# Performance work log

Measured on AMD Instinct MI355X. Metric: run time of the kernel, lower is better.

The kernel has to match this reference:

```python
import jax, jax.numpy as jnp
import numpy as np

NUM_EMBEDDINGS = 1024
EMBEDDING_DIM = 256
COMMITMENT_COST = 0.25


def setup_inputs() -> dict:
    key = jax.random.key(0)
    k1, k2 = jax.random.split(key)
    z_e = jax.random.normal(k1, (32, EMBEDDING_DIM, 32, 32), dtype=jnp.float32)
    # nn.Embedding weight init: uniform(-1/K, 1/K)
    embedding = jax.random.uniform(
        k2, (NUM_EMBEDDINGS, EMBEDDING_DIM), dtype=jnp.float32,
        minval=-1.0 / NUM_EMBEDDINGS, maxval=1.0 / NUM_EMBEDDINGS)
    return {"z_e": z_e, "embedding": embedding}


def reference(z_e, embedding):
    B, D, H, W = z_e.shape
    K = embedding.shape[0]
    sg = jax.lax.stop_gradient

    z = jnp.transpose(z_e, (0, 2, 3, 1))            # (B, H, W, D)
    flat = z.reshape(-1, D)                          # (N, D), N = B*H*W

    distances = (jnp.sum(flat * flat, axis=1, keepdims=True)
                 + jnp.sum(embedding * embedding, axis=1)
                 - 2.0 * flat @ embedding.T)

    encoding_indices = jnp.argmin(distances, axis=1)  # (N,)
    # one_hot @ embedding == direct gather of nearest code vectors
    z_q_flat = embedding[encoding_indices]            # (N, D)
    z_q = z_q_flat.reshape(z.shape)                   # (B, H, W, D)

    e_latent_loss = jnp.mean((sg(z_q) - z) ** 2)
    q_latent_loss = jnp.mean((z_q - sg(z)) ** 2)
    loss = q_latent_loss + COMMITMENT_COST * e_latent_loss

    # straight-through estimator
    z_q_st = z + sg(z_q - z)
    z_q_out = jnp.transpose(z_q_st, (0, 3, 1, 2))     # (B, D, H, W)

    # avg_probs = mean over N of one-hot == histogram of indices / N
    N = flat.shape[0]
    counts = jnp.zeros((K,), dtype=jnp.float32).at[encoding_indices].add(1.0)
    avg_probs = counts / N
    perplexity = jnp.exp(-jnp.sum(avg_probs * jnp.log(avg_probs + 1e-10)))

    return (z_q_out, loss, perplexity, encoding_indices, distances)
```

## Files before the change

### kernel.cpp

```cpp
#include <hip/hip_runtime.h>
#include <cfloat>

typedef __attribute__((ext_vector_type(8))) short bf16x8;
typedef __attribute__((ext_vector_type(4))) float f32x4;
typedef __attribute__((ext_vector_type(8))) unsigned short u16x8;

#define NROW 32768
#define ZQ_OFF   0
#define LOSS_OFF 8388608
#define PERP_OFF 8388609
#define IDX_OFF  8388610
#define DIST_OFF 8421378

#define WSB_AHI  0x0
#define WSB_BHI  0x1000000
#define WSB_RN   0x2100000
#define WSB_EN   0x2120000
#define WSB_PKEY 0x2200000
#define WSB_CNT  0x2620000
#define WSB_LOSS 0x2621000

__device__ __forceinline__ float sq_rn(float x) { return __fmul_rn(x, x); }

__device__ __forceinline__ unsigned enc_f(float f) {
  unsigned u = __float_as_uint(f);
  return (u & 0x80000000u) ? ~u : (u | 0x80000000u);
}
__device__ __forceinline__ float dec_f(unsigned e) {
  unsigned u = (e & 0x80000000u) ? (e ^ 0x80000000u) : ~e;
  return __uint_as_float(u);
}

__device__ __forceinline__ unsigned short bf16_rne(float f) {
  unsigned u = __float_as_uint(f);
  unsigned r = u + 0x7fffu + ((u >> 16) & 1u);
  return (unsigned short)(r >> 16);
}

__device__ __forceinline__ void gload16(const void* g, void* l) {
  __builtin_amdgcn_global_load_lds(
      (const __attribute__((address_space(1))) unsigned int*)g,
      (__attribute__((address_space(3))) unsigned int*)l, 16, 0, 0);
}

__device__ float pairwise_norm256(const float* __restrict__ p, int stride) {
  float h[2];
#pragma unroll
  for (int half = 0; half < 2; ++half) {
    const float* q = p + (size_t)half * 128 * stride;
    float r[8];
#pragma unroll
    for (int j = 0; j < 8; ++j) r[j] = sq_rn(q[(size_t)j * stride]);
    for (int d8 = 8; d8 < 128; d8 += 8) {
#pragma unroll
      for (int j = 0; j < 8; ++j)
        r[j] = __fadd_rn(r[j], sq_rn(q[(size_t)(d8 + j) * stride]));
    }
    h[half] = __fadd_rn(__fadd_rn(__fadd_rn(r[0], r[1]), __fadd_rn(r[2], r[3])),
                        __fadd_rn(__fadd_rn(r[4], r[5]), __fadd_rn(r[6], r[7])));
  }
  return __fadd_rn(h[0], h[1]);
}

__launch_bounds__(256)
__global__ void prep_all_kernel(const float* __restrict__ z_e,
                                const float* __restrict__ emb,
                                unsigned short* __restrict__ ahi,
                                unsigned short* __restrict__ bhi,
                                float* __restrict__ rownorm,
                                float* __restrict__ embnorm,
                                float* __restrict__ zero_region) {
  __shared__ float xt[64][132];
  __shared__ float hs[128][2];
  const int t = threadIdx.x;
  if (blockIdx.x >= 256) {
    const int bx = blockIdx.x - 256;
    if (bx >= 132) {
      for (int i = t; i < 1026; i += 256) zero_region[i] = 0.f;
      return;
    }
    if (bx >= 128) {
      const int k = ((bx - 128) << 8) + t;
      embnorm[k] = pairwise_norm256(emb + ((size_t)k << 8), 1);
      return;
    }
    const int tg = (bx << 8) + t;
    const int k = tg >> 5, cd = tg & 31;
    const float4 v0 = *(const float4*)(emb + ((size_t)k << 8) + cd * 8);
    const float4 v1 = *(const float4*)(emb + ((size_t)k << 8) + cd * 8 + 4);
    const float xs[8] = {v0.x, v0.y, v0.z, v0.w, v1.x, v1.y, v1.z, v1.w};
    u16x8 vh;
#pragma unroll
    for (int u = 0; u < 8; ++u) vh[u] = (short)bf16_rne(xs[u]);
    const size_t pos = (((size_t)(k >> 7)) << 12) + ((size_t)(cd >> 3) << 10)
                     + ((size_t)(k & 127) << 3) + (size_t)((cd & 7) ^ (k & 7));
    *(u16x8*)(bhi + pos * 8) = vh;
    return;
  }
  const int ntile = blockIdx.x;
  const int n0 = ntile << 7;
  const int b = n0 >> 10, s0 = n0 & 1023;
  const size_t zb = ((size_t)b << 18) + (size_t)s0;
  const int myhalf = t >> 7;
  const int mys = t & 127;
  float r[8];
#pragma unroll
  for (int j = 0; j < 8; ++j) r[j] = 0.f;
  for (int dt = 0; dt < 4; ++dt) {
#pragma unroll
    for (int p = 0; p < 8; ++p) {
      const int idx = (p << 8) + t;
      const int dd = idx >> 5;
      const int sq = (idx & 31) << 2;
      const float4 v = *(const float4*)(z_e + zb + ((size_t)((dt << 6) + dd) << 10) + sq);
      const int sw = ((dd >> 3) & 3) << 3;
      *(float4*)(&xt[dd][sq ^ sw]) = v;
    }
    __syncthreads();
    if ((dt >> 1) == myhalf) {
#pragma unroll
      for (int g = 0; g < 8; ++g) {
        const int col = mys ^ ((g & 3) << 3);
#pragma unroll
        for (int j = 0; j < 8; ++j)
          r[j] = __fadd_rn(r[j], sq_rn(xt[(g << 3) + j][col]));
      }
    }
#pragma unroll
    for (int p = 0; p < 4; ++p) {
      const int idx = (p << 8) + t;
      const int s = idx >> 3, c = idx & 7;
      const int sw = (c & 3) << 3;
      u16x8 vh;
#pragma unroll
      for (int u = 0; u < 8; ++u)
        vh[u] = (short)bf16_rne(xt[(c << 3) + u][s ^ sw]);
      const size_t pos = ((size_t)ntile << 12) + ((size_t)dt << 10)
                       + (size_t)(s << 3) + (size_t)(c ^ (s & 7));
      *(u16x8*)(ahi + pos * 8) = vh;
    }
    __syncthreads();
  }
  const float h = __fadd_rn(__fadd_rn(__fadd_rn(r[0], r[1]), __fadd_rn(r[2], r[3])),
                            __fadd_rn(__fadd_rn(r[4], r[5]), __fadd_rn(r[6], r[7])));
  hs[mys][myhalf] = h;
  __syncthreads();
  if (t < 128) rownorm[n0 + t] = __fadd_rn(hs[t][0], hs[t][1]);
}

#define LDS_A 0
#define LDS_B 16384

__launch_bounds__(256, 4)
__global__ void dist_kernel(const unsigned short* __restrict__ ahi,
                            const unsigned short* __restrict__ bhi,
                            const float* __restrict__ rownorm,
                            const float* __restrict__ embnorm,
                            float* __restrict__ dist,
                            unsigned long long* __restrict__ pkey) {
  __shared__ char lds[32768];
  const int tid = threadIdx.x;
  const int lane = tid & 63;
  const int wv = tid >> 6;
  const int wr = wv >> 1, wc = wv & 1;
  const int bid = blockIdx.x;
  const int xcd = bid & 7;
  const int jj = bid >> 3;
  const int ntile = (xcd << 5) + (jj >> 3);
  const int ktile = jj & 7;

  const unsigned short* gsrc = (wv < 2) ? ahi + ((size_t)ntile << 15)
                                        : bhi + ((size_t)ktile << 15);
  char* ldsBase = lds + ((wv >> 1) << 14);

  f32x4 acc[4][4];
#pragma unroll
  for (int i = 0; i < 4; ++i)
#pragma unroll
    for (int j = 0; j < 4; ++j) acc[i][j] = (f32x4){0.f, 0.f, 0.f, 0.f};

  for (int s = 0; s < 4; ++s) {
    {
      const unsigned short* g = gsrc + ((size_t)s << 13);
#pragma unroll
      for (int q = 0; q < 8; ++q) {
        const int cq = ((wv & 1) << 3) + q;
        gload16(g + ((size_t)(cq * 64 + lane) << 3), ldsBase + cq * 1024);
      }
    }
    __syncthreads();
#pragma unroll
    for (int half = 0; half < 2; ++half) {
      const int kb = half << 2;
      bf16x8 ah[4], bh[4];
#pragma unroll
      for (int i = 0; i < 4; ++i) {
        const int row = (wr << 6) + (i << 4) + (lane & 15);
        const int ch = (kb + (lane >> 4)) ^ (row & 7);
        ah[i] = *(const bf16x8*)(lds + LDS_A + ((row << 3) + ch) * 16);
      }
#pragma unroll
      for (int j = 0; j < 4; ++j) {
        const int row = (wc << 6) + (j << 4) + (lane & 15);
        const int ch = (kb + (lane >> 4)) ^ (row & 7);
        bh[j] = *(const bf16x8*)(lds + LDS_B + ((row << 3) + ch) * 16);
      }
#pragma unroll
      for (int i = 0; i < 4; ++i)
#pragma unroll
        for (int j = 0; j < 4; ++j)
          acc[i][j] = __builtin_amdgcn_mfma_f32_16x16x32_bf16(ah[i], bh[j], acc[i][j], 0, 0, 0);
    }
    __syncthreads();
  }
  const int n0 = (ntile << 7) + (wr << 6);
  const int k0 = (ktile << 7) + (wc << 6);
  const int g = lane >> 4, tl = lane & 15;
  const int tileidx = (ktile << 1) + wc;
  float en[4];
#pragma unroll
  for (int j = 0; j < 4; ++j) en[j] = embnorm[k0 + (j << 4) + tl];
#pragma unroll
  for (int i = 0; i < 4; ++i) {
#pragma unroll
    for (int r = 0; r < 4; ++r) {
      const int n = n0 + (i << 4) + (g << 2) + r;
      const float rn = rownorm[n];
      float* drow = dist + (size_t)n * 1024 + k0 + tl;
      unsigned long long key = ~0ULL;
#pragma unroll
      for (int j = 0; j < 4; ++j) {
        const float dv = __fsub_rn(__fadd_rn(rn, en[j]), __fmul_rn(2.0f, acc[i][j][r]));
        drow[j << 4] = dv;
        const unsigned long long c =
            ((unsigned long long)enc_f(dv) << 32) | (unsigned)(k0 + (j << 4) + tl);
        key = c < key ? c : key;
      }
#pragma unroll
      for (int mm = 1; mm < 16; mm <<= 1) {
        const unsigned long long o = __shfl_xor(key, mm, 64);
        key = o < key ? o : key;
      }
      if (tl == 0) pkey[(size_t)n * 16 + tileidx] = key;
    }
  }
}

__launch_bounds__(256)
__global__ void rzq_kernel(const float* __restrict__ z_e,
                           const float* __restrict__ emb,
                           const float* __restrict__ rownorm,
                           const float* __restrict__ embnorm,
                           const float* __restrict__ dist,
                           const unsigned long long* __restrict__ pkey,
                           float* __restrict__ out,
                           float* __restrict__ counts,
                           float* __restrict__ lossacc) {
  __shared__ float xl[16][260];
  __shared__ int bk_s[16];
  __shared__ float wredf[4];
  const int t = threadIdx.x;
  const int s0 = blockIdx.x << 4;
  const int b = s0 >> 10, sb = s0 & 1023;
  {
    const int d = t >> 2;
    const int s4 = (t & 3) << 2;
#pragma unroll
    for (int p = 0; p < 4; ++p) {
      const int dd = d + p * 64;
      const float4 v = *(const float4*)(z_e + ((size_t)b << 18) + ((size_t)dd << 10) + sb + s4);
      xl[s4 + 0][dd] = v.x; xl[s4 + 1][dd] = v.y;
      xl[s4 + 2][dd] = v.z; xl[s4 + 3][dd] = v.w;
    }
  }
  __syncthreads();
  const int wv = t >> 6, lane = t & 63;
  for (int rr = 0; rr < 4; ++rr) {
    const int srow = (wv << 2) + rr;
    const int n = s0 + srow;
    const unsigned long long mypk = (lane < 16) ? pkey[(size_t)n * 16 + lane] : ~0ULL;
    unsigned long long key = mypk;
#pragma unroll
    for (int mm = 1; mm < 64; mm <<= 1) {
      const unsigned long long o = __shfl_xor(key, mm, 64);
      key = o < key ? o : key;
    }
    const float v1 = dec_f((unsigned)(key >> 32));
    const unsigned ue = (__float_as_uint(v1) >> 23) & 0xffu;
    const float ulp = __uint_as_float((ue - 23) << 23);
    const float w = v1 + 2.0f * ulp + 3e-3f;
    unsigned qmask = (unsigned)(__ballot(dec_f((unsigned)(mypk >> 32)) <= w) & 0xffffULL);
    const float rn = rownorm[n];
    const float4 xv = *(const float4*)(&xl[srow][lane << 2]);
    unsigned long long best = ~0ULL;
    while (qmask) {
      const int T = __ffs(qmask) - 1;
      qmask &= qmask - 1;
      const float dval = dist[(size_t)n * 1024 + T * 64 + lane];
      unsigned long long cm = __ballot(dval <= w);
      while (cm) {
        const int l2 = __ffsll(cm) - 1;
        cm &= cm - 1;
        const int kk = T * 64 + l2;
        const float4 ev = *(const float4*)(emb + ((size_t)kk << 8) + (lane << 2));
        double p = (double)xv.x * ev.x + (double)xv.y * ev.y
                 + (double)xv.z * ev.z + (double)xv.w * ev.w;
#pragma unroll
        for (int mm = 1; mm < 64; mm <<= 1) p += __shfl_xor(p, mm, 64);
        const float dotf = (float)p;
        const float D = __fsub_rn(__fadd_rn(rn, embnorm[kk]), __fmul_rn(2.0f, dotf));
        const unsigned long long c = ((unsigned long long)enc_f(D) << 32) | (unsigned)kk;
        best = c < best ? c : best;
      }
    }
    const int bestk = (int)(best & 0xffffffffu);
    if (lane == 0) {
      bk_s[srow] = bestk;
      out[IDX_OFF + n] = (float)bestk;
      atomicAdd(&counts[bestk], 1.0f);
    }
  }
  __syncthreads();
  const int d = t;
  float zq[16];
  float lsum = 0.f;
#pragma unroll
  for (int r2 = 0; r2 < 16; ++r2) {
    const float e = emb[((size_t)bk_s[r2] << 8) + d];
    const float z = xl[r2][d];
    const float df = __fsub_rn(e, z);
    zq[r2] = __fadd_rn(z, df);
    lsum = fmaf(df, df, lsum);
  }
  float* op = out + ZQ_OFF + ((size_t)b << 18) + ((size_t)d << 10) + sb;
#pragma unroll
  for (int q = 0; q < 4; ++q)
    *(float4*)(op + (q << 2)) =
        make_float4(zq[q * 4], zq[q * 4 + 1], zq[q * 4 + 2], zq[q * 4 + 3]);
#pragma unroll
  for (int m = 32; m > 0; m >>= 1) lsum += __shfl_xor(lsum, m, 64);
  if (lane == 0) wredf[wv] = lsum;
  __syncthreads();
  if (t == 0) atomicAdd(lossacc, wredf[0] + wredf[1] + wredf[2] + wredf[3]);
}

__launch_bounds__(256)
__global__ void final_kernel(const float* __restrict__ counts, const float* __restrict__ lossacc,
                             float* __restrict__ out) {
  const int t = threadIdx.x;
  float ssum = 0.f;
#pragma unroll
  for (int u = 0; u < 4; ++u) {
    const float p = counts[t * 4 + u] * (1.0f / 32768.0f);
    ssum += p * logf(p + 1e-10f);
  }
#pragma unroll
  for (int m = 32; m > 0; m >>= 1) ssum += __shfl_xor(ssum, m, 64);
  __shared__ float wred[4];
  if ((t & 63) == 0) wred[t >> 6] = ssum;
  __syncthreads();
  if (t == 0) {
    const float tot = wred[0] + wred[1] + wred[2] + wred[3];
    out[PERP_OFF] = expf(-tot);
    const float mql = lossacc[0] * (1.0f / 8388608.0f);
    out[LOSS_OFF] = __fadd_rn(mql, __fmul_rn(0.25f, mql));
  }
}

extern "C" void kernel_launch(void* const* d_in, const int* in_sizes, int n_in,
                              void* d_out, int out_size, void* d_ws, size_t ws_size,
                              hipStream_t stream) {
  const float* z_e = (const float*)d_in[0];
  const float* emb = (const float*)d_in[1];
  float* out = (float*)d_out;
  char* ws = (char*)d_ws;

  unsigned short* ahi = (unsigned short*)(ws + WSB_AHI);
  unsigned short* bhi = (unsigned short*)(ws + WSB_BHI);
  float* rownorm = (float*)(ws + WSB_RN);
  float* embnorm = (float*)(ws + WSB_EN);
  unsigned long long* pkey = (unsigned long long*)(ws + WSB_PKEY);
  float* counts = (float*)(ws + WSB_CNT);
  float* lossacc = (float*)(ws + WSB_LOSS);

  hipLaunchKernelGGL(prep_all_kernel, dim3(389), dim3(256), 0, stream,
                     z_e, emb, ahi, bhi, rownorm, embnorm, counts);
  hipLaunchKernelGGL(dist_kernel, dim3(2048), dim3(256), 0, stream,
                     ahi, bhi, rownorm, embnorm, out + DIST_OFF, pkey);
  hipLaunchKernelGGL(rzq_kernel, dim3(2048), dim3(256), 0, stream,
                     z_e, emb, rownorm, embnorm, out + DIST_OFF, pkey, out, counts, lossacc);
  hipLaunchKernelGGL(final_kernel, dim3(1), dim3(256), 0, stream, counts, lossacc, out);
}
```

Before: 119.7 us.

## Fuse final reduction into rzq via last-block counter, halve prep tiles, nontemporal dist stores

The separate single-block final kernel is removed. The last rzq block, detected by an atomic counter, now computes perplexity and loss, which saves a launch. The prep kernel processes 64-row tiles instead of 128, doubling the block count to raise parallelism and cut per-block LDS. Distance stores become nontemporal so the large distance matrix avoids polluting cache. The counter lives at zero_region offset 1024 and is zeroed by prep, but the fused tail adds a serial atomic handshake.

```diff
diff --git a/kernel.cpp b/kernel.cpp
--- a/kernel.cpp
+++ b/kernel.cpp
@@ -19,6 +19,7 @@
 #define WSB_PKEY 0x2200000
 #define WSB_CNT  0x2620000
 #define WSB_LOSS 0x2621000
+#define WSB_CTR  0x2621004
 
 __device__ __forceinline__ float sq_rn(float x) { return __fmul_rn(x, x); }
 
@@ -70,11 +71,11 @@
                                 float* __restrict__ rownorm,
                                 float* __restrict__ embnorm,
                                 float* __restrict__ zero_region) {
-  __shared__ float xt[64][132];
-  __shared__ float hs[128][2];
+  __shared__ float xt[64][68];
+  __shared__ float hs[64][2];
   const int t = threadIdx.x;
-  if (blockIdx.x >= 256) {
-    const int bx = blockIdx.x - 256;
+  if (blockIdx.x >= 512) {
+    const int bx = blockIdx.x - 512;
     if (bx >= 132) {
       for (int i = t; i < 1026; i += 256) zero_region[i] = 0.f;
       return;
@@ -97,27 +98,29 @@
     *(u16x8*)(bhi + pos * 8) = vh;
     return;
   }
-  const int ntile = blockIdx.x;
-  const int n0 = ntile << 7;
+  const int bx = blockIdx.x;
+  const int ntile = bx >> 1;
+  const int shalf = bx & 1;
+  const int n0 = bx << 6;
   const int b = n0 >> 10, s0 = n0 & 1023;
   const size_t zb = ((size_t)b << 18) + (size_t)s0;
-  const int myhalf = t >> 7;
-  const int mys = t & 127;
+  const int mys = t & 63;
+  const int myhalf = (t >> 6) & 1;
   float r[8];
 #pragma unroll
   for (int j = 0; j < 8; ++j) r[j] = 0.f;
   for (int dt = 0; dt < 4; ++dt) {
 #pragma unroll
-    for (int p = 0; p < 8; ++p) {
+    for (int p = 0; p < 4; ++p) {
       const int idx = (p << 8) + t;
-      const int dd = idx >> 5;
-      const int sq = (idx & 31) << 2;
+      const int dd = idx >> 4;
+      const int sq = (idx & 15) << 2;
       const float4 v = *(const float4*)(z_e + zb + ((size_t)((dt << 6) + dd) << 10) + sq);
       const int sw = ((dd >> 3) & 3) << 3;
       *(float4*)(&xt[dd][sq ^ sw]) = v;
     }
     __syncthreads();
-    if ((dt >> 1) == myhalf) {
+    if (t < 128 && (dt >> 1) == myhalf) {
 #pragma unroll
       for (int g = 0; g < 8; ++g) {
         const int col = mys ^ ((g & 3) << 3);
@@ -127,25 +130,28 @@
       }
     }
 #pragma unroll
-    for (int p = 0; p < 4; ++p) {
+    for (int p = 0; p < 2; ++p) {
       const int idx = (p << 8) + t;
-      const int s = idx >> 3, c = idx & 7;
+      const int sl = idx >> 3, c = idx & 7;
       const int sw = (c & 3) << 3;
       u16x8 vh;
 #pragma unroll
       for (int u = 0; u < 8; ++u)
-        vh[u] = (short)bf16_rne(xt[(c << 3) + u][s ^ sw]);
+        vh[u] = (short)bf16_rne(xt[(c << 3) + u][sl ^ sw]);
+      const int sg = (shalf << 6) + sl;
       const size_t pos = ((size_t)ntile << 12) + ((size_t)dt << 10)
-                       + (size_t)(s << 3) + (size_t)(c ^ (s & 7));
+                       + (size_t)(sg << 3) + (size_t)(c ^ (sg & 7));
       *(u16x8*)(ahi + pos * 8) = vh;
     }
     __syncthreads();
   }
-  const float h = __fadd_rn(__fadd_rn(__fadd_rn(r[0], r[1]), __fadd_rn(r[2], r[3])),
-                            __fadd_rn(__fadd_rn(r[4], r[5]), __fadd_rn(r[6], r[7])));
-  hs[mys][myhalf] = h;
-  __syncthreads();
-  if (t < 128) rownorm[n0 + t] = __fadd_rn(hs[t][0], hs[t][1]);
+  if (t < 128) {
+    const float h = __fadd_rn(__fadd_rn(__fadd_rn(r[0], r[1]), __fadd_rn(r[2], r[3])),
+                              __fadd_rn(__fadd_rn(r[4], r[5]), __fadd_rn(r[6], r[7])));
+    hs[mys][myhalf] = h;
+  }
+  __syncthreads();
+  if (t < 64) rownorm[n0 + t] = __fadd_rn(hs[t][0], hs[t][1]);
 }
 
 #define LDS_A 0
@@ -231,7 +237,7 @@
 #pragma unroll
       for (int j = 0; j < 4; ++j) {
         const float dv = __fsub_rn(__fadd_rn(rn, en[j]), __fmul_rn(2.0f, acc[i][j][r]));
-        drow[j << 4] = dv;
+        __builtin_nontemporal_store(dv, &drow[j << 4]);
         const unsigned long long c =
             ((unsigned long long)enc_f(dv) << 32) | (unsigned)(k0 + (j << 4) + tl);
         key = c < key ? c : key;
@@ -255,10 +261,12 @@
                            const unsigned long long* __restrict__ pkey,
                            float* __restrict__ out,
                            float* __restrict__ counts,
-                           float* __restrict__ lossacc) {
+                           float* __restrict__ lossacc,
+                           unsigned* __restrict__ ctr) {
   __shared__ float xl[16][260];
   __shared__ int bk_s[16];
   __shared__ float wredf[4];
+  __shared__ unsigned lastflag;
   const int t = threadIdx.x;
   const int s0 = blockIdx.x << 4;
   const int b = s0 >> 10, sb = s0 & 1023;
@@ -321,48 +329,51 @@
     }
   }
   __syncthreads();
-  const int d = t;
-  float zq[16];
-  float lsum = 0.f;
-#pragma unroll
-  for (int r2 = 0; r2 < 16; ++r2) {
-    const float e = emb[((size_t)bk_s[r2] << 8) + d];
-    const float z = xl[r2][d];
-    const float df = __fsub_rn(e, z);
-    zq[r2] = __fadd_rn(z, df);
-    lsum = fmaf(df, df, lsum);
-  }
-  float* op = out + ZQ_OFF + ((size_t)b << 18) + ((size_t)d << 10) + sb;
-#pragma unroll
-  for (int q = 0; q < 4; ++q)
-    *(float4*)(op + (q << 2)) =
-        make_float4(zq[q * 4], zq[q * 4 + 1], zq[q * 4 + 2], zq[q * 4 + 3]);
-#pragma unroll
-  for (int m = 32; m > 0; m >>= 1) lsum += __shfl_xor(lsum, m, 64);
-  if (lane == 0) wredf[wv] = lsum;
-  __syncthreads();
-  if (t == 0) atomicAdd(lossacc, wredf[0] + wredf[1] + wredf[2] + wredf[3]);
-}
-
-__launch_bounds__(256)
-__global__ void final_kernel(const float* __restrict__ counts, const float* __restrict__ lossacc,
-                             float* __restrict__ out) {
-  const int t = threadIdx.x;
+  {
+    const int d = t;
+    float zq[16];
+    float lsum = 0.f;
+#pragma unroll
+    for (int r2 = 0; r2 < 16; ++r2) {
+      const float e = emb[((size_t)bk_s[r2] << 8) + d];
+      const float z = xl[r2][d];
+      const float df = __fsub_rn(e, z);
+      zq[r2] = __fadd_rn(z, df);
+      lsum = fmaf(df, df, lsum);
+    }
+    float* op = out + ZQ_OFF + ((size_t)b << 18) + ((size_t)d << 10) + sb;
+#pragma unroll
+    for (int q = 0; q < 4; ++q)
+      *(float4*)(op + (q << 2)) =
+          make_float4(zq[q * 4], zq[q * 4 + 1], zq[q * 4 + 2], zq[q * 4 + 3]);
+#pragma unroll
+    for (int m = 32; m > 0; m >>= 1) lsum += __shfl_xor(lsum, m, 64);
+    if (lane == 0) wredf[wv] = lsum;
+  }
+  __syncthreads();
+  if (t == 0) {
+    atomicAdd(lossacc, wredf[0] + wredf[1] + wredf[2] + wredf[3]);
+    asm volatile("s_waitcnt vmcnt(0)" ::: "memory");
+    lastflag = (atomicAdd(ctr, 1u) == 2047u) ? 1u : 0u;
+  }
+  __syncthreads();
+  if (!lastflag) return;
   float ssum = 0.f;
 #pragma unroll
   for (int u = 0; u < 4; ++u) {
-    const float p = counts[t * 4 + u] * (1.0f / 32768.0f);
+    const float cv = atomicAdd(&counts[t * 4 + u], 0.0f);
+    const float p = cv * (1.0f / 32768.0f);
     ssum += p * logf(p + 1e-10f);
   }
 #pragma unroll
   for (int m = 32; m > 0; m >>= 1) ssum += __shfl_xor(ssum, m, 64);
-  __shared__ float wred[4];
-  if ((t & 63) == 0) wred[t >> 6] = ssum;
+  __shared__ float wred2[4];
+  if ((t & 63) == 0) wred2[t >> 6] = ssum;
   __syncthreads();
   if (t == 0) {
-    const float tot = wred[0] + wred[1] + wred[2] + wred[3];
+    const float tot = wred2[0] + wred2[1] + wred2[2] + wred2[3];
     out[PERP_OFF] = expf(-tot);
-    const float mql = lossacc[0] * (1.0f / 8388608.0f);
+    const float mql = atomicAdd(lossacc, 0.0f) * (1.0f / 8388608.0f);
     out[LOSS_OFF] = __fadd_rn(mql, __fmul_rn(0.25f, mql));
   }
 }
@@ -382,12 +393,13 @@
   unsigned long long* pkey = (unsigned long long*)(ws + WSB_PKEY);
   float* counts = (float*)(ws + WSB_CNT);
   float* lossacc = (float*)(ws + WSB_LOSS);
-
-  hipLaunchKernelGGL(prep_all_kernel, dim3(389), dim3(256), 0, stream,
+  unsigned* ctr = (unsigned*)(ws + WSB_CTR);
+
+  hipLaunchKernelGGL(prep_all_kernel, dim3(645), dim3(256), 0, stream,
                      z_e, emb, ahi, bhi, rownorm, embnorm, counts);
   hipLaunchKernelGGL(dist_kernel, dim3(2048), dim3(256), 0, stream,
                      ahi, bhi, rownorm, embnorm, out + DIST_OFF, pkey);
   hipLaunchKernelGGL(rzq_kernel, dim3(2048), dim3(256), 0, stream,
-                     z_e, emb, rownorm, embnorm, out + DIST_OFF, pkey, out, counts, lossacc);
-  hipLaunchKernelGGL(final_kernel, dim3(1), dim3(256), 0, stream, counts, lossacc, out);
-}
+                     z_e, emb, rownorm, embnorm, out + DIST_OFF, pkey,
+                     out, counts, lossacc, ctr);
+}
```

New measurement: 172.3 us. 43.9% more time.
